# Kernel tuning notes

Hardware: AMD Instinct MI355X
Metric: run time of the kernel (lower is better)

Reference implementation:

```python
import jax, jax.numpy as jnp
import numpy as np

D = 1024
H = 16
HD = D // H
T = 2048
B = 2
EPS = 1e-7

def setup_inputs() -> dict:
    key = jax.random.key(0)
    ks = jax.random.split(key, 16)
    s = 0.02
    return {
        "x":  jax.random.normal(ks[0], (B, T, D), jnp.float32),
        "Wq": jax.random.normal(ks[1], (D, D), jnp.float32) * s,
        "bq": jnp.zeros((D,), jnp.float32),
        "Wk": jax.random.normal(ks[2], (D, D), jnp.float32) * s,
        "bk": jnp.zeros((D,), jnp.float32),
        "Wv": jax.random.normal(ks[3], (D, D), jnp.float32) * s,
        "bv": jnp.zeros((D,), jnp.float32),
        "Wo": jax.random.normal(ks[4], (D, D), jnp.float32) * s,
        "bo": jnp.zeros((D,), jnp.float32),
        "W1": jax.random.normal(ks[5], (D, 4 * D), jnp.float32) * s,
        "b1": jnp.zeros((4 * D,), jnp.float32),
        "W2": jax.random.normal(ks[6], (4 * D, D), jnp.float32) * s,
        "b2": jnp.zeros((D,), jnp.float32),
        "g1": jnp.ones((D,), jnp.float32),
        "be1": jnp.zeros((D,), jnp.float32),
        "g2": jnp.ones((D,), jnp.float32),
        "be2": jnp.zeros((D,), jnp.float32),
    }

def layer_norm(x, gamma, beta):
    mu = jnp.mean(x, axis=-1, keepdims=True)
    var = jnp.mean(jnp.square(x - mu), axis=-1, keepdims=True)  # biased var
    return (x - mu) / jnp.sqrt(var + EPS) * gamma + beta

def attention(x, Wq, bq, Wk, bk, Wv, bv, Wo, bo):
    b, t, d = x.shape
    q = (x @ Wq + bq).reshape(b, t, H, HD).transpose(0, 2, 1, 3)  # [B,H,T,HD]
    k = (x @ Wk + bk).reshape(b, t, H, HD).transpose(0, 2, 1, 3)
    v = (x @ Wv + bv).reshape(b, t, H, HD).transpose(0, 2, 1, 3)
    scores = jnp.einsum("bhqd,bhkd->bhqk", q, k) / np.sqrt(HD).astype(np.float32)
    causal = jnp.tril(jnp.ones((t, t), bool))
    scores = jnp.where(causal, scores, -jnp.inf)
    attn = jax.nn.softmax(scores, axis=-1)
    out = jnp.einsum("bhqk,bhkd->bhqd", attn, v)
    out = out.transpose(0, 2, 1, 3).reshape(b, t, d)
    return out @ Wo + bo

def reference(x, Wq, bq, Wk, bk, Wv, bv, Wo, bo, W1, b1, W2, b2, g1, be1, g2, be2):
    x = x + attention(layer_norm(x, g1, be1), Wq, bq, Wk, bk, Wv, bv, Wo, bo)
    h = layer_norm(x, g2, be2)
    x = x + (jax.nn.relu(h @ W1 + b1) @ W2 + b2)
    return x
```

## Files before the change

kernel.cpp:

```cpp
#include <hip/hip_runtime.h>
#include <hip/hip_bf16.h>

#define Dm 1024
#define Hn 16
#define HDm 64
#define Tm 2048
#define Bm 2
#define MR (Bm*Tm)
#define SQK 3072

typedef __attribute__((ext_vector_type(8))) short bfrag8;
typedef __attribute__((ext_vector_type(4))) float floatx4;

__device__ __forceinline__ float bf2f(ushort u){
  union { unsigned int i; float f; } c; c.i = ((unsigned int)u)<<16; return c.f;
}
__device__ __forceinline__ ushort f2bf(float f){
  unsigned int u = __float_as_uint(f);
  u += 0x7fffu + ((u>>16)&1u);
  return (ushort)(u>>16);
}
__device__ __forceinline__ void gl2lds16(const ushort* g, ushort* l){
  __builtin_amdgcn_global_load_lds(
    (const __attribute__((address_space(1))) unsigned int*)g,
    (__attribute__((address_space(3))) unsigned int*)l,
    16, 0, 0);
}
__device__ __forceinline__ int is_f32(const unsigned int* g1w){
  return *g1w == 0x3F800000u;
}

#define POFF0 (1ul*524288)
#define POFF1 (9ul*524288)
#define POFF2 (25ul*524288)
#define POFF3 (73ul*524288)

__global__ __launch_bounds__(256) void prep_vec(const void* bq, const void* bk, const void* bv,
                                                const void* bo, const void* b1, const void* b2,
                                                const void* g1, const void* be1,
                                                const void* g2, const void* be2,
                                                float* __restrict__ dst){
  int i = blockIdx.x*256 + threadIdx.x;
  if (i >= 13312) return;
  int f = is_f32((const unsigned int*)g1);
  const void* src; int off;
  if      (i < 1024)  { src = bq;  off = i; }
  else if (i < 2048)  { src = bk;  off = i-1024; }
  else if (i < 3072)  { src = bv;  off = i-2048; }
  else if (i < 4096)  { src = bo;  off = i-3072; }
  else if (i < 8192)  { src = b1;  off = i-4096; }
  else if (i < 9216)  { src = b2;  off = i-8192; }
  else if (i < 10240) { src = g1;  off = i-9216; }
  else if (i < 11264) { src = be1; off = i-10240; }
  else if (i < 12288) { src = g2;  off = i-11264; }
  else                { src = be2; off = i-12288; }
  dst[i] = f ? ((const float*)src)[off] : bf2f(((const ushort*)src)[off]);
}

__device__ __forceinline__ void transpose_body(const void* src, ushort* dst,
                                               int K, int N, int f32){
  __shared__ ushort s[32][33];
  int bx = blockIdx.x, by = blockIdx.y;
  int tx = threadIdx.x, ty = threadIdx.y;
#pragma unroll
  for(int r=0;r<4;r++){
    size_t gi = (size_t)(by*32+ty+8*r)*N + bx*32+tx;
    s[ty+8*r][tx] = f32 ? f2bf(((const float*)src)[gi]) : ((const ushort*)src)[gi];
  }
  __syncthreads();
#pragma unroll
  for(int r=0;r<4;r++)
    dst[(size_t)(bx*32+ty+8*r)*K + by*32+tx] = s[tx][ty+8*r];
}
__global__ __launch_bounds__(256) void transpose_cast(const void* __restrict__ src,
                                                      ushort* __restrict__ dst,
                                                      int K, int N, const unsigned int* g1w){
  transpose_body(src, dst, K, N, is_f32(g1w));
}
__global__ __launch_bounds__(256) void transpose_qkvo(const void* Wq, const void* Wk,
                                                      const void* Wv, const void* Wo,
                                                      ushort* __restrict__ Wqkvt,
                                                      ushort* __restrict__ Wot,
                                                      const unsigned int* g1w){
  int z = blockIdx.z;
  const void* src = (z==0)?Wq:(z==1)?Wk:(z==2)?Wv:Wo;
  ushort* dst = (z<3) ? (Wqkvt + (size_t)z*1024*1024) : Wot;
  transpose_body(src, dst, 1024, 1024, is_f32(g1w));
}

__global__ __launch_bounds__(256) void vtrans(const ushort* __restrict__ qkv,
                                              ushort* __restrict__ vt){
  __shared__ ushort s[32][33];
  int bhz = blockIdx.z;
  int bx = blockIdx.x;
  int by = blockIdx.y;
  int tx = threadIdx.x, ty = threadIdx.y;
  int b = bhz>>4, h = bhz&15;
  const ushort* src = qkv + (size_t)b*Tm*SQK + 2048 + h*64;
#pragma unroll
  for(int r=0;r<4;r++)
    s[ty+8*r][tx] = src[(size_t)(bx*32+ty+8*r)*SQK + by*32+tx];
  __syncthreads();
  ushort* dst = vt + (size_t)bhz*HDm*Tm;
#pragma unroll
  for(int r=0;r<4;r++)
    dst[(size_t)(by*32+ty+8*r)*Tm + bx*32+tx] = s[tx][ty+8*r];
}

template<int MODE>
__global__ __launch_bounds__(256) void ln_kernel(const void* __restrict__ xin,
                                                 const float* __restrict__ g,
                                                 const float* __restrict__ be,
                                                 ushort* __restrict__ out,
                                                 const unsigned int* g1w){
  int row = blockIdx.x;
  int tid = threadIdx.x;
  size_t base = (size_t)row*Dm + tid*4;
  float v[4];
  bool f32in = (MODE==1) || (MODE==0 && is_f32(g1w));
  if (f32in){
    const float4 t = *(const float4*)((const float*)xin + base);
    v[0]=t.x; v[1]=t.y; v[2]=t.z; v[3]=t.w;
  } else {
    ushort4 t = *(const ushort4*)((const ushort*)xin + base);
    v[0]=bf2f(t.x); v[1]=bf2f(t.y); v[2]=bf2f(t.z); v[3]=bf2f(t.w);
  }
  float s  = v[0]+v[1]+v[2]+v[3];
  float s2 = v[0]*v[0]+v[1]*v[1]+v[2]*v[2]+v[3]*v[3];
#pragma unroll
  for(int o=1;o<64;o<<=1){
    s  += __shfl_xor(s,  o, 64);
    s2 += __shfl_xor(s2, o, 64);
  }
  __shared__ float red[8];
  int wv = tid>>6;
  if ((tid&63)==0){ red[wv]=s; red[wv+4]=s2; }
  __syncthreads();
  s  = red[0]+red[1]+red[2]+red[3];
  s2 = red[4]+red[5]+red[6]+red[7];
  float mu  = s  * (1.0f/Dm);
  float var = s2 * (1.0f/Dm) - mu*mu;
  float rstd = rsqrtf(var + 1e-7f);
  float4 gg = *(const float4*)(g  + tid*4);
  float4 bb = *(const float4*)(be + tid*4);
  ushort4 o4;
  o4.x = f2bf((v[0]-mu)*rstd*gg.x+bb.x);
  o4.y = f2bf((v[1]-mu)*rstd*gg.y+bb.y);
  o4.z = f2bf((v[2]-mu)*rstd*gg.z+bb.z);
  o4.w = f2bf((v[3]-mu)*rstd*gg.w+bb.w);
  *(ushort4*)(out + base) = o4;
}

#define BKt 64
enum { E_BF16=0, E_RELU=1, E_OPROJ=2, E_FINALB=3, E_PARTB=4, E_PARTB4=5 };

template<int EPI>
__global__ __launch_bounds__(256) void gemm_bt(const ushort* __restrict__ A, int lda,
                                               const ushort* __restrict__ Bt, int ldb,
                                               const float* __restrict__ bias,
                                               void* __restrict__ Cout, int ldc,
                                               int Ki,
                                               const unsigned int* g1w){
  __shared__ ushort As[128*BKt];
  __shared__ ushort Bs[128*BKt];
  int tid = threadIdx.x;
  int bn, bm, zid = 0;
  if (EPI==E_BF16){
    int lin = blockIdx.y*24 + blockIdx.x;
    int xcd = lin&7, pos = lin>>3;
    bn = (xcd&1)*12 + pos%12;
    bm = (xcd>>1)*8 + pos/12;
  } else if (EPI==E_RELU){
    int lin = blockIdx.y*32 + blockIdx.x;
    int xcd = lin&7, pos = lin>>3;
    bm = (xcd&3)*8 + (pos&7);
    bn = (xcd>>2)*16 + (pos>>3);
  } else if (EPI==E_PARTB4){
    int lin = (blockIdx.z*32 + blockIdx.y)*8 + blockIdx.x;
    int xcd = lin&7, pos = lin>>3;
    zid = xcd>>1;
    bm = (xcd&1)*16 + (pos>>3);
    bn = pos&7;
  } else {
    bn = blockIdx.x; bm = blockIdx.y; zid = blockIdx.z;
  }
  int wv = tid>>6, lane = tid&63;
  int quad = lane>>4, l16 = lane&15;
  int wm = (wv&1)*64, wn = (wv>>1)*64;
  floatx4 acc[4][4] = {};
  int koff = (EPI==E_PARTB || EPI==E_PARTB4) ? zid*Ki : 0;
  const ushort* Aptr = A  + (size_t)bm*128*lda + koff;
  const ushort* Bptr = Bt + (size_t)bn*128*ldb + koff;
  int rl = lane>>3;
  int cs = ((lane&7) ^ rl)*8;

  for(int k0=0; k0<Ki; k0+=BKt){
    __syncthreads();
#pragma unroll
    for(int c=0;c<4;c++){
      gl2lds16(&Aptr[(size_t)(wv*32 + c*8 + rl)*lda + k0 + cs], &As[(wv*32 + c*8)*BKt]);
      gl2lds16(&Bptr[(size_t)(wv*32 + c*8 + rl)*ldb + k0 + cs], &Bs[(wv*32 + c*8)*BKt]);
    }
    __syncthreads();
#pragma unroll
    for(int f=0;f<2;f++){
      int sw = (((f<<2)|quad) ^ (l16&7))*8;
      bfrag8 a[4], b[4];
#pragma unroll
      for(int i=0;i<4;i++) a[i] = *(const bfrag8*)&As[(wm+i*16+l16)*BKt + sw];
#pragma unroll
      for(int j=0;j<4;j++) b[j] = *(const bfrag8*)&Bs[(wn+j*16+l16)*BKt + sw];
#pragma unroll
      for(int i=0;i<4;i++)
#pragma unroll
        for(int j=0;j<4;j++)
          acc[i][j] = __builtin_amdgcn_mfma_f32_16x16x32_bf16(a[i], b[j], acc[i][j], 0,0,0);
    }
  }

  ushort* part = (ushort*)Cout;
  if (EPI==E_PARTB)  part += (size_t)zid*MR*1024;
  if (EPI==E_PARTB4) part += (zid==0?POFF0 : zid==1?POFF1 : zid==2?POFF2 : POFF3);
#pragma unroll
  for(int i=0;i<4;i++){
    int gr = bm*128 + wm + i*16 + quad*4;
#pragma unroll
    for(int j=0;j<4;j++){
      int gc = bn*128 + wn + j*16 + l16;
      float bb = (EPI==E_PARTB || EPI==E_PARTB4) ? 0.0f : bias[gc];
#pragma unroll
      for(int rg=0; rg<4; rg++){
        size_t idx = (size_t)(gr+rg)*ldc + gc;
        float val = acc[i][j][rg] + bb;
        if (EPI==E_RELU)   part[idx] = f2bf(val>0.0f?val:0.0f);
        else               part[idx] = f2bf(val);
      }
    }
  }
}

__global__ __launch_bounds__(256) void ffn2_reduce(const ushort* __restrict__ p0,
                                                   const ushort* __restrict__ p1,
                                                   const float* __restrict__ bias,
                                                   const ushort* __restrict__ resid,
                                                   void* __restrict__ out,
                                                   const unsigned int* g1w){
  int e = (blockIdx.x*256 + threadIdx.x)*4;
  ushort4 a = *(const ushort4*)&p0[e];
  ushort4 b = *(const ushort4*)&p1[e];
  ushort4 r = *(const ushort4*)&resid[e];
  float4 bb = *(const float4*)&bias[e & 1023];
  float v0 = bf2f(a.x)+bf2f(b.x)+bb.x+bf2f(r.x);
  float v1 = bf2f(a.y)+bf2f(b.y)+bb.y+bf2f(r.y);
  float v2 = bf2f(a.z)+bf2f(b.z)+bb.z+bf2f(r.z);
  float v3 = bf2f(a.w)+bf2f(b.w)+bb.w+bf2f(r.w);
  if (is_f32(g1w)){
    float4 o = {v0,v1,v2,v3};
    *(float4*)((float*)out + e) = o;
  } else {
    ushort4 o = {f2bf(v0),f2bf(v1),f2bf(v2),f2bf(v3)};
    *(ushort4*)((ushort*)out + e) = o;
  }
}

__global__ __launch_bounds__(256) void ffn2_reduce4(const ushort* __restrict__ pb,
                                                    const float* __restrict__ bias,
                                                    const ushort* __restrict__ resid,
                                                    void* __restrict__ out,
                                                    const unsigned int* g1w){
  int e = (blockIdx.x*256 + threadIdx.x)*4;
  ushort4 a = *(const ushort4*)&pb[POFF0 + e];
  ushort4 b = *(const ushort4*)&pb[POFF1 + e];
  ushort4 c = *(const ushort4*)&pb[POFF2 + e];
  ushort4 d = *(const ushort4*)&pb[POFF3 + e];
  ushort4 r = *(const ushort4*)&resid[e];
  float4 bb = *(const float4*)&bias[e & 1023];
  float v0 = bf2f(a.x)+bf2f(b.x)+bf2f(c.x)+bf2f(d.x)+bb.x+bf2f(r.x);
  float v1 = bf2f(a.y)+bf2f(b.y)+bf2f(c.y)+bf2f(d.y)+bb.y+bf2f(r.y);
  float v2 = bf2f(a.z)+bf2f(b.z)+bf2f(c.z)+bf2f(d.z)+bb.z+bf2f(r.z);
  float v3 = bf2f(a.w)+bf2f(b.w)+bf2f(c.w)+bf2f(d.w)+bb.w+bf2f(r.w);
  if (is_f32(g1w)){
    float4 o = {v0,v1,v2,v3};
    *(float4*)((float*)out + e) = o;
  } else {
    ushort4 o = {f2bf(v0),f2bf(v1),f2bf(v2),f2bf(v3)};
    *(ushort4*)((ushort*)out + e) = o;
  }
}

template<int EPI>
__global__ __launch_bounds__(128) void gemm64_bt(const ushort* __restrict__ A, int lda,
                                                 const ushort* __restrict__ Bt, int ldb,
                                                 const float* __restrict__ bias,
                                                 const void*   __restrict__ resid,
                                                 void* __restrict__ Cout, int ldc,
                                                 int Ki,
                                                 const unsigned int* g1w){
  __shared__ ushort As[64*BKt];
  __shared__ ushort Bs[64*BKt];
  int tid = threadIdx.x;
  int id = blockIdx.x;
  int xcd = id&7, sdec = id>>3;
  int bn = sdec&15, bm = (sdec>>4)*8 + xcd;
  int wv = tid>>6, lane = tid&63;
  int quad = lane>>4, l16 = lane&15;
  int wm = wv*32;
  floatx4 acc[2][4] = {};
  const ushort* Aptr = A  + (size_t)bm*64*lda;
  const ushort* Bptr = Bt + (size_t)bn*64*ldb;
  int rl = lane>>3;
  int cs = ((lane&7) ^ rl)*8;

  for(int k0=0; k0<Ki; k0+=BKt){
    __syncthreads();
#pragma unroll
    for(int c=0;c<4;c++){
      gl2lds16(&Aptr[(size_t)(wv*32 + c*8 + rl)*lda + k0 + cs], &As[(wv*32 + c*8)*BKt]);
      gl2lds16(&Bptr[(size_t)(wv*32 + c*8 + rl)*ldb + k0 + cs], &Bs[(wv*32 + c*8)*BKt]);
    }
    __syncthreads();
#pragma unroll
    for(int f=0;f<2;f++){
      int sw = (((f<<2)|quad) ^ (l16&7))*8;
      bfrag8 a[2], b[4];
#pragma unroll
      for(int i=0;i<2;i++) a[i] = *(const bfrag8*)&As[(wm+i*16+l16)*BKt + sw];
#pragma unroll
      for(int j=0;j<4;j++) b[j] = *(const bfrag8*)&Bs[(j*16+l16)*BKt + sw];
#pragma unroll
      for(int i=0;i<2;i++)
#pragma unroll
        for(int j=0;j<4;j++)
          acc[i][j] = __builtin_amdgcn_mfma_f32_16x16x32_bf16(a[i], b[j], acc[i][j], 0,0,0);
    }
  }

  int f32 = is_f32(g1w);
#pragma unroll
  for(int i=0;i<2;i++){
    int gr = bm*64 + wm + i*16 + quad*4;
#pragma unroll
    for(int j=0;j<4;j++){
      int gc = bn*64 + j*16 + l16;
      float bb = bias[gc];
#pragma unroll
      for(int rg=0; rg<4; rg++){
        size_t idx = (size_t)(gr+rg)*ldc + gc;
        float val = acc[i][j][rg] + bb;
        if (EPI==E_OPROJ){
          float r = f32 ? ((const float*)resid)[idx] : bf2f(((const ushort*)resid)[idx]);
          ((ushort*)Cout)[idx] = f2bf(val + r);
        } else {
          float r = bf2f(((const ushort*)resid)[idx]);
          if (f32) ((float*)Cout)[idx] = val + r;
          else     ((ushort*)Cout)[idx] = f2bf(val + r);
        }
      }
    }
  }
}

#define PSTR2 136

__global__ __launch_bounds__(256) void attn_mfma(const ushort* __restrict__ qkv,
                                                 const ushort* __restrict__ vt,
                                                 ushort* __restrict__ out){
  __shared__ ushort Ks[128*64];
  __shared__ ushort Vs[64*128];
  __shared__ ushort Ps[64*PSTR2];
  int id = blockIdx.x;
  int xcd = id&7, sdec = id>>3;
  int bxp = sdec&15, hb = sdec>>4;
  int h = xcd + 8*(hb&1), b = hb>>1;
  int tid = threadIdx.x;
  int wv = tid>>6, lane = tid&63;
  int quad = lane>>4, l16 = lane&15;
  const ushort* qbase = qkv + (size_t)b*Tm*SQK + h*HDm;
  const ushort* kbase = qbase + Dm;
  const ushort* vtb   = vt + (size_t)(b*Hn+h)*HDm*Tm;
  size_t obase = (size_t)b*Tm*Dm + (size_t)h*HDm;
  int rl = lane>>3;
  int cs = ((lane&7) ^ rl)*8;
  int vrow = lane>>4;
  int l7 = l16 & 7;

  for(int half=0; half<2; half++){
    int qt = half ? (31 - bxp) : bxp;
    int qrow = qt*64 + wv*16 + l16;
    bfrag8 aq[2];
#pragma unroll
    for(int f=0;f<2;f++){
      bfrag8 raw = *(const bfrag8*)&qbase[(size_t)qrow*SQK + f*32 + quad*8];
#pragma unroll
      for(int e=0;e<8;e++) aq[f][e] = (short)f2bf(bf2f((ushort)raw[e])*0.125f);
    }

    floatx4 oacc[4] = {};
    float lacc[4] = {0.0f,0.0f,0.0f,0.0f};
    int qabs0 = qt*64 + wv*16 + quad*4;
    int nr = (qt+2)>>1;

    for(int r=0; r<nr; r++){
      __syncthreads();
#pragma unroll
      for(int c=0;c<4;c++){
        int kr0 = wv*32 + c*8;
        gl2lds16(&kbase[(size_t)(r*128 + kr0 + rl)*SQK + cs], &Ks[kr0*64]);
        int d0 = wv*16 + c*4;
        int drow = d0 + vrow;
        int gg = (lane&15) ^ (drow&7);
        gl2lds16(&vtb[(size_t)drow*Tm + r*128 + gg*8], &Vs[d0*128]);
      }
      __syncthreads();

      floatx4 s[8];
#pragma unroll
      for(int j=0;j<8;j++){
        int kr = j*16 + l16;
        int k7 = kr & 7;
        bfrag8 b0 = *(const bfrag8*)&Ks[kr*64 + ((quad     ^ k7)*8)];
        bfrag8 b1 = *(const bfrag8*)&Ks[kr*64 + (((4|quad) ^ k7)*8)];
        floatx4 z = {0.0f,0.0f,0.0f,0.0f};
        z = __builtin_amdgcn_mfma_f32_16x16x32_bf16(aq[0], b0, z, 0,0,0);
        z = __builtin_amdgcn_mfma_f32_16x16x32_bf16(aq[1], b1, z, 0,0,0);
        s[j] = z;
      }
      if (2*r+1 >= qt){
#pragma unroll
        for(int j=0;j<8;j++){
          int gk = r*128 + j*16 + l16;
#pragma unroll
          for(int rg=0;rg<4;rg++)
            if (gk > qabs0 + rg) s[j][rg] = -1.0e30f;
        }
      }

#pragma unroll
      for(int j=0;j<8;j++)
#pragma unroll
        for(int rg=0;rg<4;rg++){
          float p = __expf(s[j][rg]);
          lacc[rg] += p;
          Ps[(wv*16 + quad*4+rg)*PSTR2 + j*16 + l16] = f2bf(p);
        }

      bfrag8 ap[4];
#pragma unroll
      for(int c=0;c<4;c++)
        ap[c] = *(const bfrag8*)&Ps[(wv*16 + l16)*PSTR2 + (c*4+quad)*8];
#pragma unroll
      for(int j=0;j<4;j++){
        int dr = j*16 + l16;
        int d7 = dr & 7;
#pragma unroll
        for(int c=0;c<4;c++){
          bfrag8 bv = *(const bfrag8*)&Vs[dr*128 + (((c*4+quad) ^ d7)*8)];
          oacc[j] = __builtin_amdgcn_mfma_f32_16x16x32_bf16(ap[c], bv, oacc[j], 0,0,0);
        }
      }
    }

#pragma unroll
    for(int o=1;o<16;o<<=1)
#pragma unroll
      for(int rg=0;rg<4;rg++) lacc[rg] += __shfl_xor(lacc[rg], o, 64);
    float inv[4];
#pragma unroll
    for(int rg=0;rg<4;rg++) inv[rg] = 1.0f / lacc[rg];

#pragma unroll
    for(int j=0;j<4;j++)
#pragma unroll
      for(int rg=0;rg<4;rg++){
        int t = qt*64 + wv*16 + quad*4 + rg;
        out[obase + (size_t)t*Dm + j*16 + l16] = f2bf(oacc[j][rg] * inv[rg]);
      }
  }
}

extern "C" void kernel_launch(void* const* d_in, const int* in_sizes, int n_in,
                              void* d_out, int out_size, void* d_ws, size_t ws_size,
                              hipStream_t stream) {
  const void* x   = d_in[0];
  const void* Wq  = d_in[1];
  const void* bq  = d_in[2];
  const void* Wk  = d_in[3];
  const void* bk  = d_in[4];
  const void* Wv  = d_in[5];
  const void* bv  = d_in[6];
  const void* Wo  = d_in[7];
  const void* bo  = d_in[8];
  const void* W1  = d_in[9];
  const void* b1  = d_in[10];
  const void* W2  = d_in[11];
  const void* b2  = d_in[12];
  const void* g1  = d_in[13];
  const void* be1 = d_in[14];
  const void* g2  = d_in[15];
  const void* be2 = d_in[16];
  const unsigned int* g1w = (const unsigned int*)g1;

  char* ws = (char*)d_ws;
  const size_t MB = 1024*1024;
  float*  biasf = (float*)(ws + 65536);
  ushort* Wqkvt = (ushort*)(ws + 1*MB);
  ushort* Wot   = (ushort*)(ws + 7*MB);
  ushort* W1t   = (ushort*)(ws + 9*MB);
  ushort* W2t   = (ushort*)(ws + 17*MB);
  ushort* p0    = (ushort*)(ws + 1*MB);
  ushort* p1    = (ushort*)(ws + 9*MB);
  ushort* ln1   = (ushort*)(ws + 25*MB);
  ushort* vtb   = (ushort*)(ws + 25*MB);
  ushort* h2    = (ushort*)(ws + 25*MB);
  ushort* qkv   = (ushort*)(ws + 33*MB);
  ushort* atb   = (ushort*)(ws + 57*MB);
  ushort* x1b   = (ushort*)(ws + 65*MB);
  ushort* h1    = (ushort*)(ws + 33*MB);

  prep_vec<<<52, 256, 0, stream>>>(bq,bk,bv,bo,b1,b2,g1,be1,g2,be2, biasf);

  dim3 tb(32,8);
  transpose_qkvo<<<dim3(32,32,4), tb, 0, stream>>>(Wq, Wk, Wv, Wo, Wqkvt, Wot, g1w);
  transpose_cast<<<dim3(128,32), tb, 0, stream>>>(W1, W1t, 1024, 4096, g1w);
  transpose_cast<<<dim3(32,128), tb, 0, stream>>>(W2, W2t, 4096, 1024, g1w);

  ln_kernel<0><<<MR, 256, 0, stream>>>(x, biasf+9216, biasf+10240, ln1, g1w);

  gemm_bt<E_BF16><<<dim3(24,32), 256, 0, stream>>>(ln1, 1024, Wqkvt, 1024, biasf, qkv, SQK, 1024, g1w);

  vtrans<<<dim3(64,2,32), tb, 0, stream>>>(qkv, vtb);

  attn_mfma<<<512, 256, 0, stream>>>(qkv, vtb, atb);

  gemm64_bt<E_OPROJ><<<1024, 128, 0, stream>>>(atb, 1024, Wot, 1024, biasf+3072, x, x1b, 1024, 1024, g1w);

  ln_kernel<2><<<MR, 256, 0, stream>>>(x1b, biasf+11264, biasf+12288, h2, g1w);

  gemm_bt<E_RELU><<<dim3(32,32), 256, 0, stream>>>(h2, 1024, W1t, 1024, biasf+4096, h1, 4096, 1024, g1w);

  if (ws_size >= 82*MB){
    gemm_bt<E_PARTB4><<<dim3(8,32,4), 256, 0, stream>>>(h1, 4096, W2t, 4096, nullptr, d_ws, 1024, 1024, g1w);
    ffn2_reduce4<<<4096, 256, 0, stream>>>((const ushort*)d_ws, biasf+8192, x1b, d_out, g1w);
  } else {
    gemm_bt<E_PARTB><<<dim3(8,32,2), 256, 0, stream>>>(h1, 4096, W2t, 4096, nullptr, p0, 1024, 2048, g1w);
    ffn2_reduce<<<4096, 256, 0, stream>>>(p0, p1, biasf+8192, x1b, d_out, g1w);
  }
}
```

Measured before the change: 361.2 us.

## Replace 128x128 GEMM with 256x256 ping-pong pipelined 8-wave GEMM

Replaces the 128x128-tile, 4-wave GEMM used for the QKV, FFN1 and FFN2 projections with a 256x256-tile, 8-wave kernel. It uses 128 KB of LDS split into double-buffered A and B halves, with interleaved global-to-LDS staging, explicit vmcnt/lgkmcnt waits, barriers and s_setprio around the MFMA clusters. The larger tile raises arithmetic intensity and overlaps the loads with MFMA work. In exchange the grid is much smaller (128–256 blocks, versus 768 and 1024 before), which can under-fill the 256 CUs, and the fragile manual wait counts risk subtle races.

```diff
diff --git a/kernel.cpp b/kernel.cpp
--- a/kernel.cpp
+++ b/kernel.cpp
@@ -155,88 +155,173 @@
 enum { E_BF16=0, E_RELU=1, E_OPROJ=2, E_FINALB=3, E_PARTB=4, E_PARTB4=5 };
 
 template<int EPI>
-__global__ __launch_bounds__(256) void gemm_bt(const ushort* __restrict__ A, int lda,
-                                               const ushort* __restrict__ Bt, int ldb,
-                                               const float* __restrict__ bias,
-                                               void* __restrict__ Cout, int ldc,
-                                               int Ki,
-                                               const unsigned int* g1w){
-  __shared__ ushort As[128*BKt];
-  __shared__ ushort Bs[128*BKt];
+__global__ __launch_bounds__(512,2) void gemm256(const ushort* __restrict__ A, int lda,
+                                                 const ushort* __restrict__ Bt, int ldb,
+                                                 const float* __restrict__ bias,
+                                                 void* __restrict__ Cout, int ldc,
+                                                 int Ki,
+                                                 const unsigned int* g1w){
+  __shared__ ushort lds[65536];
   int tid = threadIdx.x;
-  int bn, bm, zid = 0;
-  if (EPI==E_BF16){
-    int lin = blockIdx.y*24 + blockIdx.x;
-    int xcd = lin&7, pos = lin>>3;
-    bn = (xcd&1)*12 + pos%12;
-    bm = (xcd>>1)*8 + pos/12;
-  } else if (EPI==E_RELU){
-    int lin = blockIdx.y*32 + blockIdx.x;
-    int xcd = lin&7, pos = lin>>3;
-    bm = (xcd&3)*8 + (pos&7);
-    bn = (xcd>>2)*16 + (pos>>3);
-  } else if (EPI==E_PARTB4){
-    int lin = (blockIdx.z*32 + blockIdx.y)*8 + blockIdx.x;
-    int xcd = lin&7, pos = lin>>3;
-    zid = xcd>>1;
-    bm = (xcd&1)*16 + (pos>>3);
-    bn = pos&7;
-  } else {
-    bn = blockIdx.x; bm = blockIdx.y; zid = blockIdx.z;
-  }
+  int lin = blockIdx.x;
+  int xcd = lin&7, pos = lin>>3;
+  int bm, bn, zid = 0;
+  if (EPI==E_BF16){        bm=(xcd&3)*4+(pos&3);  bn=(xcd>>2)*6+(pos>>2); }
+  else if (EPI==E_RELU){   bm=(xcd&3)*4+(pos&3);  bn=(xcd>>2)*8+(pos>>2); }
+  else if (EPI==E_PARTB4){ zid=xcd>>1; bm=(xcd&1)*8+(pos>>2); bn=pos&3; }
+  else {                   zid=xcd&1;  bm=(xcd>>1)*4+(pos>>2); bn=pos&3; }
   int wv = tid>>6, lane = tid&63;
   int quad = lane>>4, l16 = lane&15;
-  int wm = (wv&1)*64, wn = (wv>>1)*64;
-  floatx4 acc[4][4] = {};
-  int koff = (EPI==E_PARTB || EPI==E_PARTB4) ? zid*Ki : 0;
-  const ushort* Aptr = A  + (size_t)bm*128*lda + koff;
-  const ushort* Bptr = Bt + (size_t)bn*128*ldb + koff;
+  int wm = (wv>>2)*128, wn = (wv&3)*64;
   int rl = lane>>3;
-  int cs = ((lane&7) ^ rl)*8;
-
-  for(int k0=0; k0<Ki; k0+=BKt){
-    __syncthreads();
-#pragma unroll
-    for(int c=0;c<4;c++){
-      gl2lds16(&Aptr[(size_t)(wv*32 + c*8 + rl)*lda + k0 + cs], &As[(wv*32 + c*8)*BKt]);
-      gl2lds16(&Bptr[(size_t)(wv*32 + c*8 + rl)*ldb + k0 + cs], &Bs[(wv*32 + c*8)*BKt]);
-    }
-    __syncthreads();
-#pragma unroll
-    for(int f=0;f<2;f++){
-      int sw = (((f<<2)|quad) ^ (l16&7))*8;
-      bfrag8 a[4], b[4];
-#pragma unroll
-      for(int i=0;i<4;i++) a[i] = *(const bfrag8*)&As[(wm+i*16+l16)*BKt + sw];
-#pragma unroll
-      for(int j=0;j<4;j++) b[j] = *(const bfrag8*)&Bs[(wn+j*16+l16)*BKt + sw];
-#pragma unroll
-      for(int i=0;i<4;i++)
-#pragma unroll
-        for(int j=0;j<4;j++)
-          acc[i][j] = __builtin_amdgcn_mfma_f32_16x16x32_bf16(a[i], b[j], acc[i][j], 0,0,0);
-    }
+  int cs = ((lane&7)^rl)*8;
+  const ushort* Aptr = A  + (size_t)bm*256*lda + (size_t)zid*Ki;
+  const ushort* Bptr = Bt + (size_t)bn*256*ldb + (size_t)zid*Ki;
+  floatx4 acc[8][4] = {};
+  bfrag8 afr[4][2], bfr[4][2];
+  const int NI = Ki>>7;
+
+  auto STG = [&](ushort* dst, const ushort* g, int ld){
+    gl2lds16(&g[(size_t)(wv*16+rl)*ld + cs],   dst + (wv*16)*64);
+    gl2lds16(&g[(size_t)(wv*16+8+rl)*ld + cs], dst + (wv*16+8)*64);
+  };
+  auto LD8 = [&](const ushort* base, int r, int G)->bfrag8{
+    return *(const bfrag8*)&base[r*64 + ((G ^ (r&7))<<3)];
+  };
+#define BAR256 __builtin_amdgcn_s_barrier()
+#define LGKM0  do{ asm volatile("s_waitcnt lgkmcnt(0)" ::: "memory"); __builtin_amdgcn_sched_barrier(0);}while(0)
+#define MM256(a_,b_,c_) c_ = __builtin_amdgcn_mfma_f32_16x16x32_bf16(a_,b_,c_,0,0,0)
+
+  STG(lds+32768,      Bptr,                    ldb);
+  STG(lds+32768+8192, Bptr+(size_t)128*ldb,    ldb);
+  STG(lds,            Aptr,                    lda);
+  STG(lds+8192,       Aptr+(size_t)128*lda,    lda);
+  STG(lds+49152,      Bptr+64,                 ldb);
+  STG(lds+49152+8192, Bptr+(size_t)128*ldb+64, ldb);
+  STG(lds+16384,      Aptr+64,                 lda);
+  asm volatile("s_waitcnt vmcnt(6)" ::: "memory");
+  BAR256;
+
+  for(int i=0;i<NI;i++){
+    bool nl = (i < NI-1);
+    int kc = i*128;
+#pragma unroll
+    for(int m=0;m<4;m++){ int r=wm+m*16+l16;
+      afr[m][0]=LD8(lds, r, quad);  afr[m][1]=LD8(lds, r, 4|quad); }
+#pragma unroll
+    for(int j=0;j<4;j++){ int r=wn+j*16+l16;
+      bfr[j][0]=LD8(lds+32768, r, quad); bfr[j][1]=LD8(lds+32768, r, 4|quad); }
+    STG(lds+16384+8192, Aptr+(size_t)128*lda + kc+64, lda);
+    BAR256; LGKM0;
+    __builtin_amdgcn_s_setprio(1);
+#pragma unroll
+    for(int m=0;m<4;m++)
+#pragma unroll
+      for(int j=0;j<2;j++){ MM256(afr[m][0],bfr[j][0],acc[m][j]); MM256(afr[m][1],bfr[j][1],acc[m][j]); }
+    __builtin_amdgcn_s_setprio(0);
+    BAR256;
+    if(nl) STG(lds+32768, Bptr + kc+128, ldb);
+    BAR256;
+    __builtin_amdgcn_s_setprio(1);
+#pragma unroll
+    for(int m=0;m<4;m++)
+#pragma unroll
+      for(int j=2;j<4;j++){ MM256(afr[m][0],bfr[j][0],acc[m][j]); MM256(afr[m][1],bfr[j][1],acc[m][j]); }
+    __builtin_amdgcn_s_setprio(0);
+    BAR256;
+#pragma unroll
+    for(int m=0;m<4;m++){ int r=wm+(4+m)*16+l16;
+      afr[m][0]=LD8(lds, r, quad);  afr[m][1]=LD8(lds, r, 4|quad); }
+    if(nl) STG(lds+32768+8192, Bptr+(size_t)128*ldb + kc+128, ldb);
+    BAR256; LGKM0;
+    __builtin_amdgcn_s_setprio(1);
+#pragma unroll
+    for(int m=0;m<4;m++)
+#pragma unroll
+      for(int j=2;j<4;j++){ MM256(afr[m][0],bfr[j][0],acc[4+m][j]); MM256(afr[m][1],bfr[j][1],acc[4+m][j]); }
+    __builtin_amdgcn_s_setprio(0);
+    BAR256;
+    if(nl) STG(lds, Aptr + kc+128, lda);
+    BAR256;
+    __builtin_amdgcn_s_setprio(1);
+#pragma unroll
+    for(int m=0;m<4;m++)
+#pragma unroll
+      for(int j=0;j<2;j++){ MM256(afr[m][0],bfr[j][0],acc[4+m][j]); MM256(afr[m][1],bfr[j][1],acc[4+m][j]); }
+    __builtin_amdgcn_s_setprio(0);
+    if(nl) asm volatile("s_waitcnt vmcnt(6)" ::: "memory");
+    else   asm volatile("s_waitcnt vmcnt(0)" ::: "memory");
+    BAR256;
+#pragma unroll
+    for(int m=0;m<4;m++){ int r=wm+m*16+l16;
+      afr[m][0]=LD8(lds+16384, r, quad);  afr[m][1]=LD8(lds+16384, r, 4|quad); }
+#pragma unroll
+    for(int j=0;j<4;j++){ int r=wn+j*16+l16;
+      bfr[j][0]=LD8(lds+49152, r, quad); bfr[j][1]=LD8(lds+49152, r, 4|quad); }
+    if(nl) STG(lds+8192, Aptr+(size_t)128*lda + kc+128, lda);
+    BAR256; LGKM0;
+    __builtin_amdgcn_s_setprio(1);
+#pragma unroll
+    for(int m=0;m<4;m++)
+#pragma unroll
+      for(int j=0;j<2;j++){ MM256(afr[m][0],bfr[j][0],acc[m][j]); MM256(afr[m][1],bfr[j][1],acc[m][j]); }
+    __builtin_amdgcn_s_setprio(0);
+    BAR256;
+    if(nl) STG(lds+49152, Bptr + kc+192, ldb);
+    BAR256;
+    __builtin_amdgcn_s_setprio(1);
+#pragma unroll
+    for(int m=0;m<4;m++)
+#pragma unroll
+      for(int j=2;j<4;j++){ MM256(afr[m][0],bfr[j][0],acc[m][j]); MM256(afr[m][1],bfr[j][1],acc[m][j]); }
+    __builtin_amdgcn_s_setprio(0);
+    BAR256;
+#pragma unroll
+    for(int m=0;m<4;m++){ int r=wm+(4+m)*16+l16;
+      afr[m][0]=LD8(lds+16384, r, quad);  afr[m][1]=LD8(lds+16384, r, 4|quad); }
+    if(nl) STG(lds+49152+8192, Bptr+(size_t)128*ldb + kc+192, ldb);
+    BAR256; LGKM0;
+    __builtin_amdgcn_s_setprio(1);
+#pragma unroll
+    for(int m=0;m<4;m++)
+#pragma unroll
+      for(int j=2;j<4;j++){ MM256(afr[m][0],bfr[j][0],acc[4+m][j]); MM256(afr[m][1],bfr[j][1],acc[4+m][j]); }
+    __builtin_amdgcn_s_setprio(0);
+    BAR256;
+    if(nl) STG(lds+16384, Aptr + kc+192, lda);
+    BAR256;
+    __builtin_amdgcn_s_setprio(1);
+#pragma unroll
+    for(int m=0;m<4;m++)
+#pragma unroll
+      for(int j=0;j<2;j++){ MM256(afr[m][0],bfr[j][0],acc[4+m][j]); MM256(afr[m][1],bfr[j][1],acc[4+m][j]); }
+    __builtin_amdgcn_s_setprio(0);
+    if(nl){ asm volatile("s_waitcnt vmcnt(6)" ::: "memory"); }
+    BAR256;
   }
 
   ushort* part = (ushort*)Cout;
   if (EPI==E_PARTB)  part += (size_t)zid*MR*1024;
   if (EPI==E_PARTB4) part += (zid==0?POFF0 : zid==1?POFF1 : zid==2?POFF2 : POFF3);
 #pragma unroll
-  for(int i=0;i<4;i++){
-    int gr = bm*128 + wm + i*16 + quad*4;
+  for(int i2=0;i2<8;i2++){
+    int gr = bm*256 + wm + i2*16 + quad*4;
 #pragma unroll
     for(int j=0;j<4;j++){
-      int gc = bn*128 + wn + j*16 + l16;
+      int gc = bn*256 + wn + j*16 + l16;
       float bb = (EPI==E_PARTB || EPI==E_PARTB4) ? 0.0f : bias[gc];
 #pragma unroll
       for(int rg=0; rg<4; rg++){
         size_t idx = (size_t)(gr+rg)*ldc + gc;
-        float val = acc[i][j][rg] + bb;
-        if (EPI==E_RELU)   part[idx] = f2bf(val>0.0f?val:0.0f);
-        else               part[idx] = f2bf(val);
+        float val = acc[i2][j][rg] + bb;
+        if (EPI==E_RELU) part[idx] = f2bf(val>0.0f?val:0.0f);
+        else             part[idx] = f2bf(val);
       }
     }
   }
+#undef BAR256
+#undef LGKM0
+#undef MM256
 }
 
 __global__ __launch_bounds__(256) void ffn2_reduce(const ushort* __restrict__ p0,
@@ -526,7 +611,7 @@
 
   ln_kernel<0><<<MR, 256, 0, stream>>>(x, biasf+9216, biasf+10240, ln1, g1w);
 
-  gemm_bt<E_BF16><<<dim3(24,32), 256, 0, stream>>>(ln1, 1024, Wqkvt, 1024, biasf, qkv, SQK, 1024, g1w);
+  gemm256<E_BF16><<<192, 512, 0, stream>>>(ln1, 1024, Wqkvt, 1024, biasf, qkv, SQK, 1024, g1w);
 
   vtrans<<<dim3(64,2,32), tb, 0, stream>>>(qkv, vtb);
 
@@ -536,13 +621,13 @@
 
   ln_kernel<2><<<MR, 256, 0, stream>>>(x1b, biasf+11264, biasf+12288, h2, g1w);
 
-  gemm_bt<E_RELU><<<dim3(32,32), 256, 0, stream>>>(h2, 1024, W1t, 1024, biasf+4096, h1, 4096, 1024, g1w);
+  gemm256<E_RELU><<<256, 512, 0, stream>>>(h2, 1024, W1t, 1024, biasf+4096, h1, 4096, 1024, g1w);
 
   if (ws_size >= 82*MB){
-    gemm_bt<E_PARTB4><<<dim3(8,32,4), 256, 0, stream>>>(h1, 4096, W2t, 4096, nullptr, d_ws, 1024, 1024, g1w);
+    gemm256<E_PARTB4><<<256, 512, 0, stream>>>(h1, 4096, W2t, 4096, nullptr, d_ws, 1024, 1024, g1w);
     ffn2_reduce4<<<4096, 256, 0, stream>>>((const ushort*)d_ws, biasf+8192, x1b, d_out, g1w);
   } else {
-    gemm_bt<E_PARTB><<<dim3(8,32,2), 256, 0, stream>>>(h1, 4096, W2t, 4096, nullptr, p0, 1024, 2048, g1w);
+    gemm256<E_PARTB><<<128, 512, 0, stream>>>(h1, 4096, W2t, 4096, nullptr, p0, 1024, 2048, g1w);
     ffn2_reduce<<<4096, 256, 0, stream>>>(p0, p1, biasf+8192, x1b, d_out, g1w);
   }
 }
```

Result: faster. 337.2 us (-6.6%).
